# Performance work log

Hardware: AMD Instinct MI355X
Metric: run time of the kernel (lower is better)

The kernel has to match this reference:

```python
import jax, jax.numpy as jnp
import numpy as np

N = 20000      # nodes
E = 640000     # edges
R = 90         # relations
IN_F = 128     # raw feature dim
HID = 64       # hidden_channels
OUT = 32       # out_channels of conv2
NCLASS = 4
NB = 35        # num_bases (conv1)
EPS = 1e-16    # PyG softmax epsilon


def setup_inputs() -> dict:
    key = jax.random.key(0)
    ks = jax.random.split(key, 16)
    s = 0.1
    return {
        "x": jax.random.normal(ks[0], (N, IN_F), jnp.float32),
        "edge_index": jax.random.randint(ks[1], (2, E), 0, N, jnp.int32),
        "edge_type": jax.random.randint(ks[2], (E,), 0, R, jnp.int32),
        "edge_attr": jax.random.normal(ks[3], (E, 16), jnp.float32),
        # lin1: in_channels -> hidden (no bias)
        "lin1_w": jax.random.normal(ks[4], (IN_F, HID), jnp.float32) * s,
        # conv1: basis decomposition, heads=2, out=20, dim=2 -> H*O=40, H*dim=4
        "att1": jax.random.normal(ks[5], (R, NB), jnp.float32) * s,
        "basis1": jax.random.normal(ks[6], (NB, HID, 40), jnp.float32) * s,
        "q1": jax.random.normal(ks[7], (40, 4), jnp.float32) * s,
        "k1": jax.random.normal(ks[8], (40, 4), jnp.float32) * s,
        "wmod1": jnp.ones((20,), jnp.float32),            # mod='additive' weight (init ones)
        "bias1": jnp.zeros((80,), jnp.float32),            # concat bias: H*dim*O = 80
        # conv2: block-diagonal, in=80, blocks=2, H*O=64, H*dim=2
        "w2": jax.random.normal(ks[9], (R, 2, 40, 32), jnp.float32) * s,
        "q2": jax.random.normal(ks[10], (64, 2), jnp.float32) * s,
        "k2": jax.random.normal(ks[11], (64, 2), jnp.float32) * s,
        "lin_edge_w": jax.random.normal(ks[12], (16, 64), jnp.float32) * s,
        "e2": jax.random.normal(ks[13], (64, 2), jnp.float32) * s,
        # lin2: 2*out -> nclass
        "lin2_w": jax.random.normal(ks[14], (2 * OUT, NCLASS), jnp.float32) * s,
        "lin2_b": jnp.zeros((NCLASS,), jnp.float32),
    }


def segment_softmax(alpha, seg, num_segments):
    # PyG softmax: exp(x - detach(segment_max)) / (segment_sum + 1e-16)
    m = jax.ops.segment_max(alpha, seg, num_segments=num_segments)
    e = jnp.exp(alpha - jax.lax.stop_gradient(m)[seg])
    ssum = jax.ops.segment_sum(e, seg, num_segments=num_segments)
    return e / (ssum[seg] + EPS)


def rgat_forward(x, edge_index, edge_type, edge_attr, lin1_w, att1, basis1,
                 q1, k1, wmod1, bias1, w2, q2, k2, lin_edge_w, e2, lin2_w, lin2_b):
    src, dst = edge_index[0], edge_index[1]   # x_j = x[src], x_i = x[dst]
    n = x.shape[0]
    e = src.shape[0]

    h = x @ lin1_w                            # [N, HID]

    # ---- conv1: basis decomposition, within-relation, multiplicative attn, mod='additive'
    w = jnp.einsum('rb,bio->rio', att1, basis1)          # [R, HID, 40]
    xw = jnp.einsum('ni,rio->rno', h, w)                 # [R, N, 40] (all-relation transform)
    outj = xw[edge_type, src]                            # [E, 40]
    outi = xw[edge_type, dst]                            # [E, 40]
    qi = outi @ q1                                       # [E, 4]
    kj = outj @ k1                                       # [E, 4]
    alpha = qi * kj                                      # multiplicative-self-attention
    seg = dst.astype(jnp.int32) * R + edge_type          # within-relation softmax groups
    alpha = segment_softmax(alpha, seg, n * R)           # [E, 4]
    outj4 = outj.reshape(e, 2, 1, 20)                    # [E, H, 1, O]
    hmod = wmod1 * jnp.broadcast_to(outj4, (e, 2, 2, 20))  # mod='additive' term
    msg = outj4 * alpha.reshape(e, 2, 2, 1) + hmod       # [E, H, dim, O]
    agg = jax.ops.segment_sum(msg, dst, num_segments=n)  # [N, 2, 2, 20]
    h1 = agg.reshape(n, 80) + bias1
    h1 = jax.nn.relu(h1)

    # ---- conv2: block-diagonal, across-relation, additive attn, edge features, no bias
    xb = h1.reshape(n, 2, 40)
    xw2 = jnp.einsum('nbc,rbcd->rnbd', xb, w2).reshape(R, n, 64)  # [R, N, 64]
    outj = xw2[edge_type, src]                           # [E, 64]
    outi = xw2[edge_type, dst]
    qi = outi @ q2                                       # [E, 2]
    kj = outj @ k2
    ae = (edge_attr @ lin_edge_w) @ e2                   # [E, 2]
    alpha = jax.nn.leaky_relu(qi + kj + ae, 0.2)         # additive-self-attention
    alpha = segment_softmax(alpha, dst, n)               # across-relation
    msg = alpha.reshape(e, 2, 1) * outj.reshape(e, 2, 32)
    h2 = jax.ops.segment_sum(msg, dst, num_segments=n).reshape(n, 64)

    out = h2 @ lin2_w + lin2_b
    return jax.nn.log_softmax(out, axis=-1)


def reference(x, edge_index, edge_type, edge_attr, lin1_w, att1, basis1, q1, k1,
              wmod1, bias1, w2, q2, k2, lin_edge_w, e2, lin2_w, lin2_b):
    return rgat_forward(x, edge_index, edge_type, edge_attr, lin1_w, att1, basis1,
                        q1, k1, wmod1, bias1, w2, q2, k2, lin_edge_w, e2, lin2_w, lin2_b)
```

## Files before the change

### kernel.cpp

```cpp
#include <hip/hip_runtime.h>
#include <math.h>

constexpr int NN   = 20000;
constexpr int EE   = 640000;
constexpr int RR   = 90;
constexpr int INF_ = 128;
constexpr int HID  = 64;
constexpr float EPS = 1e-16f;
constexpr int E2   = 646144;

typedef unsigned short u16;
typedef _Float16 f16;
typedef __attribute__((ext_vector_type(8))) _Float16 f16x8;
typedef __attribute__((ext_vector_type(4))) _Float16 f16x4;
typedef __attribute__((ext_vector_type(4))) float f32x4;
typedef __attribute__((ext_vector_type(4))) int ivec4;

__device__ inline unsigned f2ord(float f) {
    unsigned u = __float_as_uint(f);
    return (u & 0x80000000u) ? ~u : (u | 0x80000000u);
}
__device__ inline float ord2f(unsigned x) {
    unsigned u = (x & 0x80000000u) ? (x & 0x7FFFFFFFu) : ~x;
    return __uint_as_float(u);
}
#define ORD_NEGINF 0x007FFFFFu

__global__ void k_fillrec(int4* p, int n) {
    int i = blockIdx.x * blockDim.x + threadIdx.x;
    if (i < n) { int4 r; r.x = 0; r.y = 0; r.z = 0; r.w = -1; p[i] = r; }
}

__global__ void k_hist(const int* et, int* hist) {
    __shared__ int lh[RR];
    if (threadIdx.x < RR) lh[threadIdx.x] = 0;
    __syncthreads();
    int i = blockIdx.x * blockDim.x + threadIdx.x;
    if (i < EE) atomicAdd(&lh[et[i]], 1);
    __syncthreads();
    if (threadIdx.x < RR) atomicAdd(&hist[threadIdx.x], lh[threadIdx.x]);
}

__global__ void k_scanPad(const int* hist, int* cursor) {
    if (threadIdx.x == 0) {
        int acc = 0;
        for (int r = 0; r < RR; ++r) {
            cursor[r] = acc;
            acc += (hist[r] + 63) & ~63;
        }
    }
}

__global__ void k_scatter(const int* src, const int* dst, const int* et,
                          int* cursor, int4* sortedR, int* posS) {
    __shared__ int lh[RR];
    __shared__ int lbase[RR];
    if (threadIdx.x < RR) lh[threadIdx.x] = 0;
    __syncthreads();
    int i = blockIdx.x * blockDim.x + threadIdx.x;
    int r = et[i];
    int rank = atomicAdd(&lh[r], 1);
    __syncthreads();
    if (threadIdx.x < RR) {
        int c = lh[threadIdx.x];
        lbase[threadIdx.x] = c ? atomicAdd(&cursor[threadIdx.x], c) : 0;
    }
    __syncthreads();
    int pos = lbase[r] + rank;
    int4 rec; rec.x = src[i]; rec.y = dst[i]; rec.z = r; rec.w = i;
    sortedR[pos] = rec;
    posS[i] = pos;
}

__global__ void k_histD(const int* dst, int* histD) {
    int i = blockIdx.x * blockDim.x + threadIdx.x;
    if (i < EE) atomicAdd(&histD[dst[i]], 1);
}

__global__ void k_scanD(const int* histD, int* rowptrD, int* cursorD) {
    __shared__ int part[256];
    const int CH = (NN + 255) / 256;
    int tid = threadIdx.x;
    int base = tid * CH;
    int s = 0;
    for (int j = 0; j < CH; ++j) {
        int idx = base + j;
        if (idx < NN) s += histD[idx];
    }
    part[tid] = s;
    __syncthreads();
    if (tid == 0) {
        int acc = 0;
        for (int t = 0; t < 256; ++t) { int v = part[t]; part[t] = acc; acc += v; }
    }
    __syncthreads();
    int acc = part[tid];
    for (int j = 0; j < CH; ++j) {
        int idx = base + j;
        if (idx < NN) {
            rowptrD[idx] = acc;
            cursorD[idx] = acc;
            acc += histD[idx];
        }
    }
    if (tid == 0) rowptrD[NN] = EE;
}

__global__ void k_scatterD(int4* sortedR, int* cursorD, u16* relD) {
    int i = blockIdx.x * blockDim.x + threadIdx.x;
    if (i >= E2) return;
    int4 rec = sortedR[i];
    if (rec.w < 0) return;
    int pos = atomicAdd(&cursorD[rec.y], 1);
    ((int*)(sortedR + i))[3] = pos;
    relD[pos] = (u16)rec.z;
}

__global__ void k_w1(const float* att1, const float* basis1, float* w1) {
    int idx = blockIdx.x * blockDim.x + threadIdx.x;
    if (idx >= RR * 2560) return;
    int r = idx / 2560, co = idx - r * 2560;
    float acc = 0.f;
    for (int b = 0; b < 35; ++b) acc += att1[r * 35 + b] * basis1[b * 2560 + co];
    w1[idx] = acc;
}

__global__ void k_wqk1(const float* w1, const float* q1, const float* k1,
                       float* wq1, float* wk1) {
    int idx = blockIdx.x * blockDim.x + threadIdx.x;
    if (idx >= RR * 64 * 4) return;
    int t = idx & 3, c = (idx >> 2) & 63, r = idx >> 8;
    const float* wrow = w1 + (size_t)r * 2560 + c * 40;
    float aq = 0.f, ak = 0.f;
    for (int o = 0; o < 40; ++o) {
        float w = wrow[o];
        aq += w * q1[o * 4 + t];
        ak += w * k1[o * 4 + t];
    }
    wq1[idx] = aq; wk1[idx] = ak;
}

__global__ void k_wqk2(const float* w2, const float* q2, const float* k2,
                       float* wq2, float* wk2) {
    int idx = blockIdx.x * blockDim.x + threadIdx.x;
    if (idx >= RR * 80 * 2) return;
    int t = idx & 1, bc = (idx >> 1) % 80, r = idx / 160;
    int b = bc / 40, c = bc % 40;
    const float* wbase = w2 + (size_t)((r * 2 + b) * 40 + c) * 32;
    float aq = 0.f, ak = 0.f;
    for (int d = 0; d < 32; ++d) {
        float w = wbase[d];
        aq += w * q2[(b * 32 + d) * 2 + t];
        ak += w * k2[(b * 32 + d) * 2 + t];
    }
    wq2[idx] = aq; wk2[idx] = ak;
}

__global__ void k_we(const float* lew, const float* e2, float* we) {
    int idx = threadIdx.x;
    if (idx >= 32) return;
    int i = idx >> 1, t = idx & 1;
    float acc = 0.f;
    for (int j = 0; j < 64; ++j) acc += lew[i * 64 + j] * e2[j * 2 + t];
    we[idx] = acc;
}

__global__ __launch_bounds__(256) void k_ae(const float* ea, const float* weg,
                                            const int* posS, float* aeS) {
    __shared__ float wes[32];
    if (threadIdx.x < 32) wes[threadIdx.x] = weg[threadIdx.x];
    __syncthreads();
    int e = blockIdx.x * 256 + threadIdx.x;
    if (e >= EE) return;
    const float4* ep = (const float4*)(ea + (size_t)e * 16);
    float a0 = 0.f, a1 = 0.f;
#pragma unroll
    for (int cc = 0; cc < 4; ++cc) {
        float4 v = ep[cc];
        const float* vv = (const float*)&v;
#pragma unroll
        for (int j = 0; j < 4; ++j) {
            int ii = cc * 4 + j;
            a0 = fmaf(vv[j], wes[ii * 2 + 0], a0);
            a1 = fmaf(vv[j], wes[ii * 2 + 1], a1);
        }
    }
    float2 av; av.x = a0; av.y = a1;
    *(float2*)(aeS + (size_t)posS[e] * 2) = av;
}

__global__ void k_w1hT(const float* w1, f16* w1hT) {
    int idx = blockIdx.x * blockDim.x + threadIdx.x;
    if (idx >= RR * 48 * 64) return;
    int k = idx & 63, o = (idx >> 6) % 48, r = idx / (48 * 64);
    float v = (o < 40) ? w1[(size_t)r * 2560 + k * 40 + o] : 0.f;
    w1hT[idx] = (f16)v;
}

__global__ void k_w2hT(const float* w2, f16* w2hT) {
    int idx = blockIdx.x * blockDim.x + threadIdx.x;
    if (idx >= RR * 2 * 32 * 64) return;
    int c = idx & 63, d = (idx >> 6) & 31, b = (idx >> 11) & 1, r = idx >> 12;
    float v = (c < 40) ? w2[((((size_t)r * 2 + b) * 40) + c) * 32 + d] : 0.f;
    w2hT[idx] = (f16)v;
}

__global__ void k_h(const float* x, const float* lin1_w, f16* hh) {
    __shared__ float xs[INF_];
    int n = blockIdx.x, t = threadIdx.x;
    xs[t]      = x[(size_t)n * INF_ + t];
    xs[t + 64] = x[(size_t)n * INF_ + t + 64];
    __syncthreads();
    float acc = 0.f;
    for (int i = 0; i < INF_; ++i) acc += xs[i] * lin1_w[i * HID + t];
    hh[(size_t)n * HID + t] = (f16)acc;
}

__global__ __launch_bounds__(256) void k_c1(const int4* sortedR, const f16* hh,
                                            const f16* w1hT,
                                            const float* wq1g, const float* wk1g,
                                            float* alpha1s, f16* outj1h) {
    __shared__ float qs[4][256], ks[4][256];
    int wid = threadIdx.x >> 6, l = threadIdx.x & 63;
    int wbase = blockIdx.x * 256 + wid * 64;
    int r = sortedR[wbase].z;
    float* qw = qs[wid];
    float* kw = ks[wid];
    for (int t = l; t < 256; t += 64) {
        qw[t] = wq1g[(size_t)r * 256 + t];
        kw[t] = wk1g[(size_t)r * 256 + t];
    }
    __syncthreads();
    int row16 = l & 15, g = l >> 4;
    f16x8 a[3][2];
#pragma unroll
    for (int mt = 0; mt < 3; ++mt)
#pragma unroll
        for (int kk = 0; kk < 2; ++kk)
            a[mt][kk] = *(const f16x8*)(w1hT + ((size_t)r * 48 + mt * 16 + row16) * 64 + kk * 32 + g * 8);
    ivec4 er[2];
    f16x8 vb0[2], vb1[2], vd0[2], vd1[2];

#define C1_LOAD(SLOT, T) { \
    int e0_ = wbase + (T) * 16; \
    er[SLOT] = __builtin_nontemporal_load((const ivec4*)(sortedR + e0_ + row16)); \
    int s_ = er[SLOT][0], d_ = er[SLOT][1]; \
    vb0[SLOT] = *(const f16x8*)(hh + (size_t)s_ * 64 + g * 8); \
    vb1[SLOT] = *(const f16x8*)(hh + (size_t)s_ * 64 + 32 + g * 8); \
    vd0[SLOT] = *(const f16x8*)(hh + (size_t)d_ * 64 + g * 8); \
    vd1[SLOT] = *(const f16x8*)(hh + (size_t)d_ * 64 + 32 + g * 8); }

#define C1_COMP(SLOT) { \
    int pd_ = er[SLOT][3]; \
    float qi[4] = {0.f,0.f,0.f,0.f}, kj[4] = {0.f,0.f,0.f,0.f}; \
    _Pragma("unroll") for (int j = 0; j < 8; ++j) { \
        int p0 = g * 8 + j, p1 = 32 + g * 8 + j; \
        float dv0 = (float)vd0[SLOT][j], dv1 = (float)vd1[SLOT][j]; \
        float bv0 = (float)vb0[SLOT][j], bv1 = (float)vb1[SLOT][j]; \
        _Pragma("unroll") for (int t2 = 0; t2 < 4; ++t2) { \
            qi[t2] = fmaf(dv0, qw[p0 * 4 + t2], fmaf(dv1, qw[p1 * 4 + t2], qi[t2])); \
            kj[t2] = fmaf(bv0, kw[p0 * 4 + t2], fmaf(bv1, kw[p1 * 4 + t2], kj[t2])); } } \
    _Pragma("unroll") for (int t2 = 0; t2 < 4; ++t2) { \
        qi[t2] += __shfl_xor(qi[t2], 16); qi[t2] += __shfl_xor(qi[t2], 32); \
        kj[t2] += __shfl_xor(kj[t2], 16); kj[t2] += __shfl_xor(kj[t2], 32); } \
    f32x4 acc[3]; \
    _Pragma("unroll") for (int mt = 0; mt < 3; ++mt) acc[mt] = (f32x4){0.f,0.f,0.f,0.f}; \
    _Pragma("unroll") for (int mt = 0; mt < 3; ++mt) { \
        acc[mt] = __builtin_amdgcn_mfma_f32_16x16x32_f16(a[mt][0], vb0[SLOT], acc[mt], 0, 0, 0); \
        acc[mt] = __builtin_amdgcn_mfma_f32_16x16x32_f16(a[mt][1], vb1[SLOT], acc[mt], 0, 0, 0); } \
    if (pd_ >= 0) { \
        if (l < 16) { \
            float4 av; \
            av.x = qi[0] * kj[0]; av.y = qi[1] * kj[1]; \
            av.z = qi[2] * kj[2]; av.w = qi[3] * kj[3]; \
            *(float4*)(alpha1s + (size_t)pd_ * 4) = av; } \
        f16* orow = outj1h + (size_t)pd_ * 40; \
        _Pragma("unroll") for (int mt = 0; mt < 3; ++mt) { \
            int col = mt * 16 + g * 4; \
            if (col < 40) { \
                f16x4 v; \
                v[0] = (f16)acc[mt][0]; v[1] = (f16)acc[mt][1]; \
                v[2] = (f16)acc[mt][2]; v[3] = (f16)acc[mt][3]; \
                *(f16x4*)(orow + col) = v; } } } }

    C1_LOAD(0, 0)
    C1_LOAD(1, 1)
    C1_COMP(0)
    C1_LOAD(0, 2)
    C1_COMP(1)
    C1_LOAD(1, 3)
    C1_COMP(0)
    C1_COMP(1)
#undef C1_LOAD
#undef C1_COMP
}

__global__ __launch_bounds__(256) void k_aggr1(const u16* relD, const int* rowptrD,
                                               const f16* outj1h, const float* alpha1s,
                                               const float* wmod, const float* bias1,
                                               f16* h1h) {
    __shared__ unsigned smax[4][RR * 5];
    __shared__ float    ssum[4][RR * 5];
    int wid = threadIdx.x >> 6;
    int lane = threadIdx.x & 63;
    int w = blockIdx.x * 4 + wid;
    int beg = rowptrD[w], end = rowptrD[w + 1];
    unsigned* mx = smax[wid];
    float*    sm = ssum[wid];
    for (int j = beg + lane; j < end; j += 64) {
        int rb = relD[j] * 5;
        mx[rb + 0] = ORD_NEGINF; mx[rb + 1] = ORD_NEGINF;
        mx[rb + 2] = ORD_NEGINF; mx[rb + 3] = ORD_NEGINF;
        sm[rb + 0] = 0.f; sm[rb + 1] = 0.f; sm[rb + 2] = 0.f; sm[rb + 3] = 0.f;
    }
    __syncthreads();
    for (int j = beg + lane; j < end; j += 64) {
        float4 a = *(const float4*)(alpha1s + (size_t)j * 4);
        int rb = relD[j] * 5;
        atomicMax(&mx[rb + 0], f2ord(a.x));
        atomicMax(&mx[rb + 1], f2ord(a.y));
        atomicMax(&mx[rb + 2], f2ord(a.z));
        atomicMax(&mx[rb + 3], f2ord(a.w));
    }
    __syncthreads();
    for (int j = beg + lane; j < end; j += 64) {
        float4 a = *(const float4*)(alpha1s + (size_t)j * 4);
        int rb = relD[j] * 5;
        atomicAdd(&sm[rb + 0], __expf(a.x - ord2f(mx[rb + 0])));
        atomicAdd(&sm[rb + 1], __expf(a.y - ord2f(mx[rb + 1])));
        atomicAdd(&sm[rb + 2], __expf(a.z - ord2f(mx[rb + 2])));
        atomicAdd(&sm[rb + 3], __expf(a.w - ord2f(mx[rb + 3])));
    }
    __syncthreads();
    for (int t = lane; t < RR * 5; t += 64) sm[t] = 1.f / (sm[t] + EPS);
    __syncthreads();
    int hh2 = lane >= 20 ? 1 : 0;
    int oo = lane - hh2 * 20;
    float acc0 = 0.f, acc1 = 0.f, accw = 0.f;
    if (lane < 40) {
        for (int j = beg; j < end; ++j) {
            int rb = relD[j] * 5 + hh2 * 2;
            float v = (float)__builtin_nontemporal_load(outj1h + (size_t)j * 40 + lane);
            float2 a = *(const float2*)(alpha1s + (size_t)j * 4 + hh2 * 2);
            float e0 = __expf(a.x - ord2f(mx[rb]));
            float e1 = __expf(a.y - ord2f(mx[rb + 1]));
            acc0 = fmaf(v, e0 * sm[rb], acc0);
            acc1 = fmaf(v, e1 * sm[rb + 1], acc1);
            accw += v;
        }
        float wm = wmod[oo];
        int b0 = hh2 * 40 + oo;
        float o0 = fmaxf(acc0 + wm * accw + bias1[b0], 0.f);
        float o1 = fmaxf(acc1 + wm * accw + bias1[b0 + 20], 0.f);
        h1h[(size_t)w * 80 + b0]      = (f16)o0;
        h1h[(size_t)w * 80 + b0 + 20] = (f16)o1;
    }
}

__global__ __launch_bounds__(256) void k_c2(const int4* sortedR, const f16* h1h,
                                            const f16* w2hT,
                                            const float* wq2g, const float* wk2g,
                                            const float* aeS,
                                            float* alpha2s, f16* outj2h) {
    __shared__ float qs[4][160], ks[4][160];
    int wid = threadIdx.x >> 6, l = threadIdx.x & 63;
    int wbase = blockIdx.x * 256 + wid * 64;
    int r = sortedR[wbase].z;
    float* qw = qs[wid];
    float* kw = ks[wid];
    for (int t = l; t < 160; t += 64) {
        qw[t] = wq2g[(size_t)r * 160 + t];
        kw[t] = wk2g[(size_t)r * 160 + t];
    }
    __syncthreads();
    int row16 = l & 15, g = l >> 4;
    f16x8 a[2][2][2];
#pragma unroll
    for (int b = 0; b < 2; ++b)
#pragma unroll
        for (int mt = 0; mt < 2; ++mt)
#pragma unroll
            for (int kk = 0; kk < 2; ++kk)
                a[b][mt][kk] = *(const f16x8*)(w2hT + ((((size_t)r * 2 + b) * 32) + mt * 16 + row16) * 64 + kk * 32 + g * 8);
    ivec4 er[2];
    f16x8 vb[2][2][2], vd[2][2][2];

#define C2_LOAD(SLOT, T) { \
    int e0_ = wbase + (T) * 16; \
    er[SLOT] = __builtin_nontemporal_load((const ivec4*)(sortedR + e0_ + row16)); \
    int s_ = er[SLOT][0], d_ = er[SLOT][1]; \
    _Pragma("unroll") for (int b = 0; b < 2; ++b) \
        _Pragma("unroll") for (int kk = 0; kk < 2; ++kk) { \
            vb[SLOT][b][kk] = *(const f16x8*)(h1h + (size_t)s_ * 80 + b * 40 + kk * 32 + g * 8); \
            vd[SLOT][b][kk] = *(const f16x8*)(h1h + (size_t)d_ * 80 + b * 40 + kk * 32 + g * 8); } }

#define C2_COMP(SLOT, T) { \
    int pd_ = er[SLOT][3]; \
    float a0 = 0.f, a1 = 0.f; \
    _Pragma("unroll") for (int b = 0; b < 2; ++b) { \
        _Pragma("unroll") for (int j = 0; j < 8; ++j) { \
            int p = b * 40 + g * 8 + j; \
            float dv = (float)vd[SLOT][b][0][j], bv = (float)vb[SLOT][b][0][j]; \
            a0 = fmaf(dv, qw[p * 2 + 0], fmaf(bv, kw[p * 2 + 0], a0)); \
            a1 = fmaf(dv, qw[p * 2 + 1], fmaf(bv, kw[p * 2 + 1], a1)); } \
        if (g == 0) { \
            _Pragma("unroll") for (int j = 0; j < 8; ++j) { \
                int p = b * 40 + 32 + j; \
                float dv = (float)vd[SLOT][b][1][j], bv = (float)vb[SLOT][b][1][j]; \
                a0 = fmaf(dv, qw[p * 2 + 0], fmaf(bv, kw[p * 2 + 0], a0)); \
                a1 = fmaf(dv, qw[p * 2 + 1], fmaf(bv, kw[p * 2 + 1], a1)); } } } \
    a0 += __shfl_xor(a0, 16); a0 += __shfl_xor(a0, 32); \
    a1 += __shfl_xor(a1, 16); a1 += __shfl_xor(a1, 32); \
    f32x4 acc[2][2]; \
    _Pragma("unroll") for (int b = 0; b < 2; ++b) \
        _Pragma("unroll") for (int mt = 0; mt < 2; ++mt) acc[b][mt] = (f32x4){0.f,0.f,0.f,0.f}; \
    _Pragma("unroll") for (int b = 0; b < 2; ++b) \
        _Pragma("unroll") for (int mt = 0; mt < 2; ++mt) { \
            acc[b][mt] = __builtin_amdgcn_mfma_f32_16x16x32_f16(a[b][mt][0], vb[SLOT][b][0], acc[b][mt], 0, 0, 0); \
            acc[b][mt] = __builtin_amdgcn_mfma_f32_16x16x32_f16(a[b][mt][1], vb[SLOT][b][1], acc[b][mt], 0, 0, 0); } \
    if (pd_ >= 0) { \
        if (l < 16) { \
            float2 aev = *(const float2*)(aeS + (size_t)(wbase + (T) * 16 + row16) * 2); \
            float x0 = a0 + aev.x, x1 = a1 + aev.y; \
            x0 = x0 > 0.f ? x0 : 0.2f * x0; \
            x1 = x1 > 0.f ? x1 : 0.2f * x1; \
            float2 av; av.x = x0; av.y = x1; \
            *(float2*)(alpha2s + (size_t)pd_ * 2) = av; } \
        f16* orow = outj2h + (size_t)pd_ * 64; \
        _Pragma("unroll") for (int b = 0; b < 2; ++b) \
            _Pragma("unroll") for (int mt = 0; mt < 2; ++mt) { \
                f16x4 v; \
                v[0] = (f16)acc[b][mt][0]; v[1] = (f16)acc[b][mt][1]; \
                v[2] = (f16)acc[b][mt][2]; v[3] = (f16)acc[b][mt][3]; \
                *(f16x4*)(orow + b * 32 + mt * 16 + g * 4) = v; } } }

    C2_LOAD(0, 0)
    C2_LOAD(1, 1)
    C2_COMP(0, 0)
    C2_LOAD(0, 2)
    C2_COMP(1, 1)
    C2_LOAD(1, 3)
    C2_COMP(0, 2)
    C2_COMP(1, 3)
#undef C2_LOAD
#undef C2_COMP
}

__global__ __launch_bounds__(256) void k_aggr2(const int* rowptrD, const f16* outj2h,
                                               const float* alpha2s, float* h2) {
    int w = blockIdx.x * 4 + (threadIdx.x >> 6);
    int lane = threadIdx.x & 63;
    if (w >= NN) return;
    int beg = rowptrD[w], end = rowptrD[w + 1];
    float m0 = -INFINITY, m1 = -INFINITY;
    for (int j = beg + lane; j < end; j += 64) {
        float2 a = *(const float2*)(alpha2s + (size_t)j * 2);
        m0 = fmaxf(m0, a.x); m1 = fmaxf(m1, a.y);
    }
#pragma unroll
    for (int off = 32; off; off >>= 1) {
        m0 = fmaxf(m0, __shfl_xor(m0, off));
        m1 = fmaxf(m1, __shfl_xor(m1, off));
    }
    float s0 = 0.f, s1 = 0.f;
    for (int j = beg + lane; j < end; j += 64) {
        float2 a = *(const float2*)(alpha2s + (size_t)j * 2);
        s0 += __expf(a.x - m0); s1 += __expf(a.y - m1);
    }
#pragma unroll
    for (int off = 32; off; off >>= 1) {
        s0 += __shfl_xor(s0, off);
        s1 += __shfl_xor(s1, off);
    }
    int b = lane >> 5;
    float mb = b ? m1 : m0;
    float rs = 1.f / ((b ? s1 : s0) + EPS);
    float acc = 0.f;
    for (int j = beg; j < end; ++j) {
        float v = (float)__builtin_nontemporal_load(outj2h + (size_t)j * 64 + lane);
        float a = alpha2s[(size_t)j * 2 + b];
        acc = fmaf(v, __expf(a - mb) * rs, acc);
    }
    h2[(size_t)w * 64 + lane] = acc;
}

__global__ void k_out(const float* h2, const float* lin2_w, const float* lin2_b,
                      float* out) {
    int n = blockIdx.x * blockDim.x + threadIdx.x;
    if (n >= NN) return;
    float o[4] = {lin2_b[0], lin2_b[1], lin2_b[2], lin2_b[3]};
    const float* hr = h2 + (size_t)n * 64;
    for (int c = 0; c < 64; ++c) {
        float hv = hr[c];
#pragma unroll
        for (int t = 0; t < 4; ++t) o[t] = fmaf(hv, lin2_w[c * 4 + t], o[t]);
    }
    float m = fmaxf(fmaxf(o[0], o[1]), fmaxf(o[2], o[3]));
    float s = __expf(o[0] - m) + __expf(o[1] - m) + __expf(o[2] - m) + __expf(o[3] - m);
    float lse = m + logf(s);
#pragma unroll
    for (int t = 0; t < 4; ++t) out[(size_t)n * 4 + t] = o[t] - lse;
}

extern "C" void kernel_launch(void* const* d_in, const int* in_sizes, int n_in,
                              void* d_out, int out_size, void* d_ws, size_t ws_size,
                              hipStream_t stream) {
    const float* x        = (const float*)d_in[0];
    const int*   eidx     = (const int*)d_in[1];
    const int*   etype    = (const int*)d_in[2];
    const float* eattr    = (const float*)d_in[3];
    const float* lin1_w   = (const float*)d_in[4];
    const float* att1     = (const float*)d_in[5];
    const float* basis1   = (const float*)d_in[6];
    const float* q1       = (const float*)d_in[7];
    const float* k1       = (const float*)d_in[8];
    const float* wmod1    = (const float*)d_in[9];
    const float* bias1    = (const float*)d_in[10];
    const float* w2       = (const float*)d_in[11];
    const float* q2       = (const float*)d_in[12];
    const float* k2       = (const float*)d_in[13];
    const float* lew      = (const float*)d_in[14];
    const float* e2i      = (const float*)d_in[15];
    const float* lin2_w   = (const float*)d_in[16];
    const float* lin2_b   = (const float*)d_in[17];

    const int* src = eidx;
    const int* dst = eidx + EE;

    float* W = (float*)d_ws;
    float* w1      = W;   W += 230400;
    float* wq1     = W;   W += 23040;
    float* wk1     = W;   W += 23040;
    float* wq2     = W;   W += 14400;
    float* wk2     = W;   W += 14400;
    float* we      = W;   W += 32;
    float* h2      = W;   W += (size_t)NN * 64;
    float* aeS     = W;   W += (size_t)E2 * 2;
    f16*   hh      = (f16*)W;   W += (size_t)NN * 64 / 2;
    f16*   h1h     = (f16*)W;   W += (size_t)NN * 80 / 2 + 32;
    f16*   w1hT    = (f16*)W;   W += (size_t)RR * 48 * 64 / 2;
    f16*   w2hT    = (f16*)W;   W += (size_t)RR * 2 * 32 * 64 / 2;
    float* uni     = W;   W += (size_t)EE * 20 + (size_t)EE * 4;
    f16*   outj1h  = (f16*)uni;
    float* alpha1s = uni + (size_t)EE * 20;
    f16*   outj2h  = (f16*)uni;
    W += (size_t)EE * 8;
    float* alpha2s = W;   W += (size_t)EE * 2;
    int4*  sortedR = (int4*)W;
    int*   I = (int*)W;   I += (size_t)E2 * 4;
    u16*   relD    = (u16*)I;   I += (size_t)E2 / 2;
    int*   posS    = I;   I += EE;
    int*   rowptrD = I;   I += NN + 1;
    int*   cursorD = I;   I += NN;
    int*   histD   = I;   I += NN;
    int*   hist    = I;   I += 128;
    int*   cursor  = I;   I += 128;

    hipMemsetAsync(histD, 0, (size_t)(NN + 256) * 4, stream);
    hipMemsetAsync(h1h + (size_t)NN * 80, 0, 128, stream);
    k_fillrec<<<E2 / 256, 256, 0, stream>>>(sortedR, E2);

    k_hist<<<EE / 256, 256, 0, stream>>>(etype, hist);
    k_scanPad<<<1, 64, 0, stream>>>(hist, cursor);
    k_scatter<<<EE / 256, 256, 0, stream>>>(src, dst, etype, cursor, sortedR, posS);
    k_histD<<<EE / 256, 256, 0, stream>>>(dst, histD);
    k_scanD<<<1, 256, 0, stream>>>(histD, rowptrD, cursorD);
    k_scatterD<<<E2 / 256, 256, 0, stream>>>(sortedR, cursorD, relD);

    k_w1<<<(RR * 2560 + 255) / 256, 256, 0, stream>>>(att1, basis1, w1);
    k_wqk1<<<(RR * 256 + 255) / 256, 256, 0, stream>>>(w1, q1, k1, wq1, wk1);
    k_wqk2<<<(RR * 160 + 255) / 256, 256, 0, stream>>>(w2, q2, k2, wq2, wk2);
    k_we<<<1, 32, 0, stream>>>(lew, e2i, we);
    k_ae<<<EE / 256, 256, 0, stream>>>(eattr, we, posS, aeS);
    k_w1hT<<<(RR * 48 * 64) / 256, 256, 0, stream>>>(w1, w1hT);
    k_w2hT<<<(RR * 2 * 32 * 64) / 256, 256, 0, stream>>>(w2, w2hT);
    k_h<<<NN, 64, 0, stream>>>(x, lin1_w, hh);

    k_c1<<<E2 / 256, 256, 0, stream>>>(sortedR, hh, w1hT, wq1, wk1, alpha1s, outj1h);
    k_aggr1<<<NN / 4, 256, 0, stream>>>(relD, rowptrD, outj1h, alpha1s,
                                        wmod1, bias1, h1h);

    k_c2<<<E2 / 256, 256, 0, stream>>>(sortedR, h1h, w2hT, wq2, wk2, aeS,
                                       alpha2s, outj2h);
    k_aggr2<<<(NN + 3) / 4, 256, 0, stream>>>(rowptrD, outj2h, alpha2s, h2);

    k_out<<<(NN + 255) / 256, 256, 0, stream>>>(h2, lin2_w, lin2_b, (float*)d_out);
}
```

Baseline: 588.0 us.

## Precompute per-relation per-node q/k projections instead of per-edge dot products

```diff
diff --git a/kernel.cpp b/kernel.cpp
--- a/kernel.cpp
+++ b/kernel.cpp
@@ -216,22 +216,78 @@
     hh[(size_t)n * HID + t] = (f16)acc;
 }
 
+__global__ __launch_bounds__(256) void k_qk1(const f16* hh, const float* wq1g,
+                                             const float* wk1g,
+                                             float* qi1, float* kj1) {
+    __shared__ float qw[256], kw[256];
+    const int nb = (NN + 63) / 64;
+    int r = blockIdx.x / nb;
+    int n0 = (blockIdx.x % nb) * 64;
+    qw[threadIdx.x] = wq1g[(size_t)r * 256 + threadIdx.x];
+    kw[threadIdx.x] = wk1g[(size_t)r * 256 + threadIdx.x];
+    __syncthreads();
+    int nl = threadIdx.x & 63, tt = threadIdx.x >> 6;
+    int n = n0 + nl;
+    if (n >= NN) return;
+    const f16x8* hp = (const f16x8*)(hh + (size_t)n * 64);
+    float aq = 0.f, ak = 0.f;
+#pragma unroll
+    for (int cc = 0; cc < 8; ++cc) {
+        f16x8 hv = hp[cc];
+#pragma unroll
+        for (int j = 0; j < 8; ++j) {
+            float h = (float)hv[j];
+            int c = cc * 8 + j;
+            aq = fmaf(h, qw[c * 4 + tt], aq);
+            ak = fmaf(h, kw[c * 4 + tt], ak);
+        }
+    }
+    qi1[((size_t)r * NN + n) * 4 + tt] = aq;
+    kj1[((size_t)r * NN + n) * 4 + tt] = ak;
+}
+
+__global__ __launch_bounds__(256) void k_qk2(const f16* h1h, const float* wq2g,
+                                             const float* wk2g,
+                                             float* qi2, float* kj2) {
+    __shared__ float qw[160], kw[160];
+    const int nb = (NN + 127) / 128;
+    int r = blockIdx.x / nb;
+    int n0 = (blockIdx.x % nb) * 128;
+    if (threadIdx.x < 160) {
+        qw[threadIdx.x] = wq2g[(size_t)r * 160 + threadIdx.x];
+        kw[threadIdx.x] = wk2g[(size_t)r * 160 + threadIdx.x];
+    }
+    __syncthreads();
+    int nl = threadIdx.x & 127, tt = threadIdx.x >> 7;
+    int n = n0 + nl;
+    if (n >= NN) return;
+    const f16x8* hp = (const f16x8*)(h1h + (size_t)n * 80);
+    float aq = 0.f, ak = 0.f;
+#pragma unroll
+    for (int cc = 0; cc < 10; ++cc) {
+        f16x8 hv = hp[cc];
+#pragma unroll
+        for (int j = 0; j < 8; ++j) {
+            float h = (float)hv[j];
+            int p = cc * 8 + j;
+            aq = fmaf(h, qw[p * 2 + tt], aq);
+            ak = fmaf(h, kw[p * 2 + tt], ak);
+        }
+    }
+    qi2[((size_t)r * NN + n) * 2 + tt] = aq;
+    kj2[((size_t)r * NN + n) * 2 + tt] = ak;
+}
+
 __global__ __launch_bounds__(256) void k_c1(const int4* sortedR, const f16* hh,
                                             const f16* w1hT,
-                                            const float* wq1g, const float* wk1g,
+                                            const float* qi1, const float* kj1,
                                             float* alpha1s, f16* outj1h) {
-    __shared__ float qs[4][256], ks[4][256];
     int wid = threadIdx.x >> 6, l = threadIdx.x & 63;
     int wbase = blockIdx.x * 256 + wid * 64;
     int r = sortedR[wbase].z;
-    float* qw = qs[wid];
-    float* kw = ks[wid];
-    for (int t = l; t < 256; t += 64) {
-        qw[t] = wq1g[(size_t)r * 256 + t];
-        kw[t] = wk1g[(size_t)r * 256 + t];
-    }
-    __syncthreads();
     int row16 = l & 15, g = l >> 4;
+    const float* qit = qi1 + (size_t)r * NN * 4;
+    const float* kjt = kj1 + (size_t)r * NN * 4;
     f16x8 a[3][2];
 #pragma unroll
     for (int mt = 0; mt < 3; ++mt)
@@ -239,7 +295,8 @@
         for (int kk = 0; kk < 2; ++kk)
             a[mt][kk] = *(const f16x8*)(w1hT + ((size_t)r * 48 + mt * 16 + row16) * 64 + kk * 32 + g * 8);
     ivec4 er[2];
-    f16x8 vb0[2], vb1[2], vd0[2], vd1[2];
+    f16x8 vb0[2], vb1[2];
+    float4 qk[2], kv[2];
 
 #define C1_LOAD(SLOT, T) { \
     int e0_ = wbase + (T) * 16; \
@@ -247,22 +304,12 @@
     int s_ = er[SLOT][0], d_ = er[SLOT][1]; \
     vb0[SLOT] = *(const f16x8*)(hh + (size_t)s_ * 64 + g * 8); \
     vb1[SLOT] = *(const f16x8*)(hh + (size_t)s_ * 64 + 32 + g * 8); \
-    vd0[SLOT] = *(const f16x8*)(hh + (size_t)d_ * 64 + g * 8); \
-    vd1[SLOT] = *(const f16x8*)(hh + (size_t)d_ * 64 + 32 + g * 8); }
+    if (g == 0) { \
+        qk[SLOT] = *(const float4*)(qit + (size_t)d_ * 4); \
+        kv[SLOT] = *(const float4*)(kjt + (size_t)s_ * 4); } }
 
 #define C1_COMP(SLOT) { \
     int pd_ = er[SLOT][3]; \
-    float qi[4] = {0.f,0.f,0.f,0.f}, kj[4] = {0.f,0.f,0.f,0.f}; \
-    _Pragma("unroll") for (int j = 0; j < 8; ++j) { \
-        int p0 = g * 8 + j, p1 = 32 + g * 8 + j; \
-        float dv0 = (float)vd0[SLOT][j], dv1 = (float)vd1[SLOT][j]; \
-        float bv0 = (float)vb0[SLOT][j], bv1 = (float)vb1[SLOT][j]; \
-        _Pragma("unroll") for (int t2 = 0; t2 < 4; ++t2) { \
-            qi[t2] = fmaf(dv0, qw[p0 * 4 + t2], fmaf(dv1, qw[p1 * 4 + t2], qi[t2])); \
-            kj[t2] = fmaf(bv0, kw[p0 * 4 + t2], fmaf(bv1, kw[p1 * 4 + t2], kj[t2])); } } \
-    _Pragma("unroll") for (int t2 = 0; t2 < 4; ++t2) { \
-        qi[t2] += __shfl_xor(qi[t2], 16); qi[t2] += __shfl_xor(qi[t2], 32); \
-        kj[t2] += __shfl_xor(kj[t2], 16); kj[t2] += __shfl_xor(kj[t2], 32); } \
     f32x4 acc[3]; \
     _Pragma("unroll") for (int mt = 0; mt < 3; ++mt) acc[mt] = (f32x4){0.f,0.f,0.f,0.f}; \
     _Pragma("unroll") for (int mt = 0; mt < 3; ++mt) { \
@@ -271,8 +318,8 @@
     if (pd_ >= 0) { \
         if (l < 16) { \
             float4 av; \
-            av.x = qi[0] * kj[0]; av.y = qi[1] * kj[1]; \
-            av.z = qi[2] * kj[2]; av.w = qi[3] * kj[3]; \
+            av.x = qk[SLOT].x * kv[SLOT].x; av.y = qk[SLOT].y * kv[SLOT].y; \
+            av.z = qk[SLOT].z * kv[SLOT].z; av.w = qk[SLOT].w * kv[SLOT].w; \
             *(float4*)(alpha1s + (size_t)pd_ * 4) = av; } \
         f16* orow = outj1h + (size_t)pd_ * 40; \
         _Pragma("unroll") for (int mt = 0; mt < 3; ++mt) { \
@@ -359,21 +406,15 @@
 
 __global__ __launch_bounds__(256) void k_c2(const int4* sortedR, const f16* h1h,
                                             const f16* w2hT,
-                                            const float* wq2g, const float* wk2g,
+                                            const float* qi2, const float* kj2,
                                             const float* aeS,
                                             float* alpha2s, f16* outj2h) {
-    __shared__ float qs[4][160], ks[4][160];
     int wid = threadIdx.x >> 6, l = threadIdx.x & 63;
     int wbase = blockIdx.x * 256 + wid * 64;
     int r = sortedR[wbase].z;
-    float* qw = qs[wid];
-    float* kw = ks[wid];
-    for (int t = l; t < 160; t += 64) {
-        qw[t] = wq2g[(size_t)r * 160 + t];
-        kw[t] = wk2g[(size_t)r * 160 + t];
-    }
-    __syncthreads();
     int row16 = l & 15, g = l >> 4;
+    const float* qit = qi2 + (size_t)r * NN * 2;
+    const float* kjt = kj2 + (size_t)r * NN * 2;
     f16x8 a[2][2][2];
 #pragma unroll
     for (int b = 0; b < 2; ++b)
@@ -383,34 +424,23 @@
             for (int kk = 0; kk < 2; ++kk)
                 a[b][mt][kk] = *(const f16x8*)(w2hT + ((((size_t)r * 2 + b) * 32) + mt * 16 + row16) * 64 + kk * 32 + g * 8);
     ivec4 er[2];
-    f16x8 vb[2][2][2], vd[2][2][2];
+    f16x8 vb[2][2][2];
+    float2 qk[2], kv[2], ae2[2];
 
 #define C2_LOAD(SLOT, T) { \
     int e0_ = wbase + (T) * 16; \
     er[SLOT] = __builtin_nontemporal_load((const ivec4*)(sortedR + e0_ + row16)); \
     int s_ = er[SLOT][0], d_ = er[SLOT][1]; \
     _Pragma("unroll") for (int b = 0; b < 2; ++b) \
-        _Pragma("unroll") for (int kk = 0; kk < 2; ++kk) { \
+        _Pragma("unroll") for (int kk = 0; kk < 2; ++kk) \
             vb[SLOT][b][kk] = *(const f16x8*)(h1h + (size_t)s_ * 80 + b * 40 + kk * 32 + g * 8); \
-            vd[SLOT][b][kk] = *(const f16x8*)(h1h + (size_t)d_ * 80 + b * 40 + kk * 32 + g * 8); } }
-
-#define C2_COMP(SLOT, T) { \
+    if (g == 0) { \
+        qk[SLOT]  = *(const float2*)(qit + (size_t)d_ * 2); \
+        kv[SLOT]  = *(const float2*)(kjt + (size_t)s_ * 2); \
+        ae2[SLOT] = *(const float2*)(aeS + (size_t)(e0_ + row16) * 2); } }
+
+#define C2_COMP(SLOT) { \
     int pd_ = er[SLOT][3]; \
-    float a0 = 0.f, a1 = 0.f; \
-    _Pragma("unroll") for (int b = 0; b < 2; ++b) { \
-        _Pragma("unroll") for (int j = 0; j < 8; ++j) { \
-            int p = b * 40 + g * 8 + j; \
-            float dv = (float)vd[SLOT][b][0][j], bv = (float)vb[SLOT][b][0][j]; \
-            a0 = fmaf(dv, qw[p * 2 + 0], fmaf(bv, kw[p * 2 + 0], a0)); \
-            a1 = fmaf(dv, qw[p * 2 + 1], fmaf(bv, kw[p * 2 + 1], a1)); } \
-        if (g == 0) { \
-            _Pragma("unroll") for (int j = 0; j < 8; ++j) { \
-                int p = b * 40 + 32 + j; \
-                float dv = (float)vd[SLOT][b][1][j], bv = (float)vb[SLOT][b][1][j]; \
-                a0 = fmaf(dv, qw[p * 2 + 0], fmaf(bv, kw[p * 2 + 0], a0)); \
-                a1 = fmaf(dv, qw[p * 2 + 1], fmaf(bv, kw[p * 2 + 1], a1)); } } } \
-    a0 += __shfl_xor(a0, 16); a0 += __shfl_xor(a0, 32); \
-    a1 += __shfl_xor(a1, 16); a1 += __shfl_xor(a1, 32); \
     f32x4 acc[2][2]; \
     _Pragma("unroll") for (int b = 0; b < 2; ++b) \
         _Pragma("unroll") for (int mt = 0; mt < 2; ++mt) acc[b][mt] = (f32x4){0.f,0.f,0.f,0.f}; \
@@ -420,8 +450,8 @@
             acc[b][mt] = __builtin_amdgcn_mfma_f32_16x16x32_f16(a[b][mt][1], vb[SLOT][b][1], acc[b][mt], 0, 0, 0); } \
     if (pd_ >= 0) { \
         if (l < 16) { \
-            float2 aev = *(const float2*)(aeS + (size_t)(wbase + (T) * 16 + row16) * 2); \
-            float x0 = a0 + aev.x, x1 = a1 + aev.y; \
+            float x0 = qk[SLOT].x + kv[SLOT].x + ae2[SLOT].x; \
+            float x1 = qk[SLOT].y + kv[SLOT].y + ae2[SLOT].y; \
             x0 = x0 > 0.f ? x0 : 0.2f * x0; \
             x1 = x1 > 0.f ? x1 : 0.2f * x1; \
             float2 av; av.x = x0; av.y = x1; \
@@ -436,12 +466,12 @@
 
     C2_LOAD(0, 0)
     C2_LOAD(1, 1)
-    C2_COMP(0, 0)
+    C2_COMP(0)
     C2_LOAD(0, 2)
-    C2_COMP(1, 1)
+    C2_COMP(1)
     C2_LOAD(1, 3)
-    C2_COMP(0, 2)
-    C2_COMP(1, 3)
+    C2_COMP(0)
+    C2_COMP(1)
 #undef C2_LOAD
 #undef C2_COMP
 }
@@ -546,6 +576,11 @@
     f16*   outj2h  = (f16*)uni;
     W += (size_t)EE * 8;
     float* alpha2s = W;   W += (size_t)EE * 2;
+    float* qkt     = W;   W += (size_t)RR * NN * 8;
+    float* qi1t    = qkt;
+    float* kj1t    = qkt + (size_t)RR * NN * 4;
+    float* qi2t    = qkt;
+    float* kj2t    = qkt + (size_t)RR * NN * 2;
     int4*  sortedR = (int4*)W;
     int*   I = (int*)W;   I += (size_t)E2 * 4;
     u16*   relD    = (u16*)I;   I += (size_t)E2 / 2;
@@ -576,11 +611,14 @@
     k_w2hT<<<(RR * 2 * 32 * 64) / 256, 256, 0, stream>>>(w2, w2hT);
     k_h<<<NN, 64, 0, stream>>>(x, lin1_w, hh);
 
-    k_c1<<<E2 / 256, 256, 0, stream>>>(sortedR, hh, w1hT, wq1, wk1, alpha1s, outj1h);
+    k_qk1<<<RR * ((NN + 63) / 64), 256, 0, stream>>>(hh, wq1, wk1, qi1t, kj1t);
+    k_c1<<<E2 / 256, 256, 0, stream>>>(sortedR, hh, w1hT, qi1t, kj1t,
+                                       alpha1s, outj1h);
     k_aggr1<<<NN / 4, 256, 0, stream>>>(relD, rowptrD, outj1h, alpha1s,
                                         wmod1, bias1, h1h);
 
-    k_c2<<<E2 / 256, 256, 0, stream>>>(sortedR, h1h, w2hT, wq2, wk2, aeS,
+    k_qk2<<<RR * ((NN + 127) / 128), 256, 0, stream>>>(h1h, wq2, wk2, qi2t, kj2t);
+    k_c2<<<E2 / 256, 256, 0, stream>>>(sortedR, h1h, w2hT, qi2t, kj2t, aeS,
                                        alpha2s, outj2h);
     k_aggr2<<<(NN + 3) / 4, 256, 0, stream>>>(rowptrD, outj2h, alpha2s, h2);
 
```

After: 743.1 us. +26.4%, slower.
